# Optimization experiments

Measured on AMD Instinct MI355X. Metric: run time of the kernel, lower is better.

## Reference

```python
import jax, jax.numpy as jnp
import numpy as np

K = 10  # num_neighbors in original nn_index call


def setup_inputs() -> dict:
    key = jax.random.key(0)
    k1, k2, k3, k4 = jax.random.split(key, 4)
    B, OBS, ACT, N = 256, 32, 2, 500000
    obs = jax.random.normal(k1, (B, OBS), dtype=jnp.float32)
    action = jax.random.normal(k2, (B, ACT), dtype=jnp.float32)
    mem_sa = jax.random.normal(k3, (N, OBS + ACT), dtype=jnp.float32)
    mem_Q = jax.random.normal(k4, (N, 1), dtype=jnp.float32)
    return {"obs": obs, "action": action, "mem_sa": mem_sa, "mem_Q": mem_Q}


def reference(obs, action, mem_sa, mem_Q):
    # query: [B, D] state-action, brute-force kNN over memory table [N, D]
    q = jnp.concatenate([obs, action], axis=1)
    # squared Euclidean distances (FLANN returns squared L2): [B, N]
    d2 = (jnp.sum(q * q, axis=1, keepdims=True)
          - 2.0 * q @ mem_sa.T
          + jnp.sum(mem_sa * mem_sa, axis=1)[None, :])
    neg_d, idx = jax.lax.top_k(-d2, K)   # nearest K neighbors
    dists = -neg_d                        # [B, K], ascending
    Qs = mem_Q[idx, 0]                    # gather Q values: [B, K]
    # NOTE: original applies softmax to raw distances (not negated)
    weights = jax.nn.softmax(dists, axis=1)
    return jnp.sum(weights * Qs, axis=1)  # [B]
```

## Files before the change

### kernel.cpp

```cpp
#include <hip/hip_runtime.h>
#include <hip/hip_bf16.h>
#include <math.h>

#define NPTS   500000
#define NB     256
#define TOPK   10
#define CAP    2048
#define SBLK   1024
#define SPER   16
#define MARGIN 2.0f
#define NWCH   15625
#define FBLK   512
#define NSEG   2
#define LCAP   8
#define PMAIN  393216
#define OCAP   32768

typedef short v2s  __attribute__((ext_vector_type(2)));
typedef short v4s  __attribute__((ext_vector_type(4)));
typedef short v8s  __attribute__((ext_vector_type(8)));
typedef float v16f __attribute__((ext_vector_type(16)));

__device__ __forceinline__ unsigned short f2bf(float f) {
    unsigned u = __float_as_uint(f);
    unsigned r = u + 0x7FFFu + ((u >> 16) & 1u);
    return (unsigned short)(r >> 16);
}
__device__ __forceinline__ float bf2f(unsigned short h) {
    return __uint_as_float(((unsigned)h) << 16);
}
__device__ __forceinline__ v2s pk2(float2 f) {
    __hip_bfloat162 h = __float22bfloat162_rn(f);
    v2s r;
    __builtin_memcpy(&r, &h, 4);
    return r;
}

__device__ __forceinline__ float norm34(const float* __restrict__ r) {
    float a0 = 0.f, a1 = 0.f, a2 = 0.f, a3 = 0.f;
#pragma unroll
    for (int d = 0; d < 32; d += 4) {
        a0 = fmaf(r[d + 0], r[d + 0], a0);
        a1 = fmaf(r[d + 1], r[d + 1], a1);
        a2 = fmaf(r[d + 2], r[d + 2], a2);
        a3 = fmaf(r[d + 3], r[d + 3], a3);
    }
    a0 = fmaf(r[32], r[32], a0);
    a1 = fmaf(r[33], r[33], a1);
    return (a0 + a1) + (a2 + a3);
}
__device__ __forceinline__ float dot34(const float* __restrict__ r, const float* q) {
    float a0 = 0.f, a1 = 0.f, a2 = 0.f, a3 = 0.f;
#pragma unroll
    for (int d = 0; d < 32; d += 4) {
        a0 = fmaf(r[d + 0], q[d + 0], a0);
        a1 = fmaf(r[d + 1], q[d + 1], a1);
        a2 = fmaf(r[d + 2], q[d + 2], a2);
        a3 = fmaf(r[d + 3], q[d + 3], a3);
    }
    a0 = fmaf(r[32], q[32], a0);
    a1 = fmaf(r[33], q[33], a1);
    return (a0 + a1) + (a2 + a3);
}
__device__ __forceinline__ float dot34_v4(const float4* __restrict__ r4, const float* q) {
    float a0 = 0.f, a1 = 0.f, a2 = 0.f, a3 = 0.f;
#pragma unroll
    for (int dp = 0; dp < 8; ++dp) {
        float4 v = r4[dp];
        a0 = fmaf(v.x, q[4 * dp + 0], a0);
        a1 = fmaf(v.y, q[4 * dp + 1], a1);
        a2 = fmaf(v.z, q[4 * dp + 2], a2);
        a3 = fmaf(v.w, q[4 * dp + 3], a3);
    }
    float2 t = *(const float2*)(r4 + 8);
    a0 = fmaf(t.x, q[32], a0);
    a1 = fmaf(t.y, q[33], a1);
    return (a0 + a1) + (a2 + a3);
}
__device__ __forceinline__ void load_q(const float* __restrict__ obs,
                                       const float* __restrict__ act, int b, float* q) {
#pragma unroll
    for (int d = 0; d < 32; ++d) q[d] = obs[b * 32 + d];
    q[32] = act[b * 2 + 0];
    q[33] = act[b * 2 + 1];
}
__device__ __forceinline__ void load9(float2* __restrict__ e,
                                      const float* __restrict__ rp, int half) {
    e[0] = *(const float2*)(rp + half * 8 + 0);
    e[1] = *(const float2*)(rp + half * 8 + 2);
    e[2] = *(const float2*)(rp + half * 8 + 4);
    e[3] = *(const float2*)(rp + half * 8 + 6);
    e[4] = *(const float2*)(rp + 16 + half * 8 + 0);
    e[5] = *(const float2*)(rp + 16 + half * 8 + 2);
    e[6] = *(const float2*)(rp + 16 + half * 8 + 4);
    e[7] = *(const float2*)(rp + 16 + half * 8 + 6);
    e[8] = *(const float2*)(rp + 32);
}

__global__ __launch_bounds__(256, 4) void k_sample(const float* __restrict__ obs,
                                                   const float* __restrict__ act,
                                                   const float* __restrict__ msa,
                                                   float* __restrict__ minima) {
    __shared__ __align__(16) float sm[SPER * 36];
    __shared__ float smn[SPER];
    const int g = blockIdx.x, t = threadIdx.x;
    const int base = g * SPER;
    for (int i = t; i < SPER * 34; i += 256) {
        int row = i / 34, d = i - row * 34;
        sm[row * 36 + d] = msa[(size_t)base * 34 + i];
    }
    __syncthreads();
    if (t < SPER) smn[t] = norm34(&sm[t * 36]);
    __syncthreads();
    float q[34];
    load_q(obs, act, t, q);
    float best = __builtin_inff();
#pragma unroll
    for (int j = 0; j < SPER; ++j) {
        float s = fmaf(-2.f, dot34_v4((const float4*)&sm[j * 36], q), smn[j]);
        best = fminf(best, s);
    }
    minima[(size_t)t * SBLK + g] = best;
}

__global__ __launch_bounds__(64) void k_tau(const float* __restrict__ minima,
                                            const float* __restrict__ obs,
                                            const float* __restrict__ act,
                                            v8s* __restrict__ afrag,
                                            int* __restrict__ cursor) {
    __shared__ __align__(16) unsigned short qs[48];
    const int b = blockIdx.x, lane = threadIdx.x;
    if (b == 0 && lane == 0) { cursor[0] = 0; cursor[1] = 0; }
    float v[16];
#pragma unroll
    for (int k = 0; k < 16; ++k) v[k] = minima[(size_t)b * SBLK + lane + 64 * k];
    float last = 0.f;
    for (int r = 0; r < TOPK; ++r) {
        float lm = v[0]; int la = 0;
#pragma unroll
        for (int k = 1; k < 16; ++k) { if (v[k] < lm) { lm = v[k]; la = k; } }
        float wm = lm;
        for (int off = 32; off; off >>= 1) wm = fminf(wm, __shfl_xor(wm, off));
        unsigned long long msk = __ballot(lm == wm);
        int first = (int)__builtin_ctzll(msk);
        if (lane == first) {
#pragma unroll
            for (int k = 0; k < 16; ++k) { if (k == la) v[k] = __builtin_inff(); }
        }
        last = wm;
    }
    float val = 0.f;
    if (lane < 32)       val = obs[b * 32 + lane];
    else if (lane < 34)  val = act[b * 2 + (lane - 32)];
    else if (lane == 34) val = -0.5f;
    else if (lane == 35) val = 0.5f * (last + MARGIN);
    if (lane < 48) qs[lane] = (lane < 36) ? f2bf(val) : (unsigned short)0;
    __syncthreads();
    if (lane < 6) {
        int s = lane >> 1, half = lane & 1;
        int qt = b >> 5, mrow = b & 31;
        v8s frag = *(const v8s*)&qs[s * 16 + half * 8];
        afrag[(qt * 3 + s) * 64 + half * 32 + mrow] = frag;
    }
}

__global__ __launch_bounds__(256, 2) void k_filter(const float* __restrict__ msa,
                                                   const v8s* __restrict__ afrag,
                                                   int* __restrict__ cursor,
                                                   unsigned* __restrict__ pbuf,
                                                   int* __restrict__ posq) {
    __shared__ int lcount[NB];
    __shared__ int lcand[NB * LCAP];
    __shared__ int gbase;
    const int g = blockIdx.x, t = threadIdx.x;
    const int w = t >> 6, lane = t & 63;
    const int mrow = lane & 31, half = lane >> 5;
    v8s A[8][3];
#pragma unroll
    for (int qt = 0; qt < 8; ++qt)
#pragma unroll
        for (int s = 0; s < 3; ++s)
            A[qt][s] = afrag[(qt * 3 + s) * 64 + lane];
    lcount[t] = 0;
    __syncthreads();
    const v16f zacc = (v16f)0.0f;
    const int gw = g * 4 + w;
    const int step = FBLK * 4;

    auto process = [&](const float2* c, int wc) {
        const int p0 = wc * 32 + mrow;
        float n0 = 0.f, n1 = 0.f;
        n0 = fmaf(c[0].x, c[0].x, n0); n1 = fmaf(c[0].y, c[0].y, n1);
        n0 = fmaf(c[1].x, c[1].x, n0); n1 = fmaf(c[1].y, c[1].y, n1);
        n0 = fmaf(c[2].x, c[2].x, n0); n1 = fmaf(c[2].y, c[2].y, n1);
        n0 = fmaf(c[3].x, c[3].x, n0); n1 = fmaf(c[3].y, c[3].y, n1);
        n0 = fmaf(c[4].x, c[4].x, n0); n1 = fmaf(c[4].y, c[4].y, n1);
        n0 = fmaf(c[5].x, c[5].x, n0); n1 = fmaf(c[5].y, c[5].y, n1);
        n0 = fmaf(c[6].x, c[6].x, n0); n1 = fmaf(c[6].y, c[6].y, n1);
        n0 = fmaf(c[7].x, c[7].x, n0); n1 = fmaf(c[7].y, c[7].y, n1);
        float part = n0 + n1;
        part = fmaf(c[8].x, c[8].x * 0.5f, part);
        part = fmaf(c[8].y, c[8].y * 0.5f, part);
        float nrm = part + __shfl_xor(part, 32);
        float thr = 0.5f * nrm;
        v4s b0lo = __builtin_shufflevector(pk2(c[0]), pk2(c[1]), 0, 1, 2, 3);
        v4s b0hi = __builtin_shufflevector(pk2(c[2]), pk2(c[3]), 0, 1, 2, 3);
        v8s B0 = __builtin_shufflevector(b0lo, b0hi, 0, 1, 2, 3, 4, 5, 6, 7);
        v4s b1lo = __builtin_shufflevector(pk2(c[4]), pk2(c[5]), 0, 1, 2, 3);
        v4s b1hi = __builtin_shufflevector(pk2(c[6]), pk2(c[7]), 0, 1, 2, 3);
        v8s B1 = __builtin_shufflevector(b1lo, b1hi, 0, 1, 2, 3, 4, 5, 6, 7);
        v8s B2 = (v8s)(short)0;
        if (half == 0) {
            v2s m33 = pk2(c[8]);
            B2[0] = m33[0];
            B2[1] = m33[1];
            B2[3] = (short)0x3F80;
        }
#pragma unroll
        for (int qt = 0; qt < 8; ++qt) {
            v16f acc = __builtin_amdgcn_mfma_f32_32x32x16_bf16(A[qt][0], B0, zacc, 0, 0, 0);
            acc = __builtin_amdgcn_mfma_f32_32x32x16_bf16(A[qt][1], B1, acc, 0, 0, 0);
            acc = __builtin_amdgcn_mfma_f32_32x32x16_bf16(A[qt][2], B2, acc, 0, 0, 0);
            float m0 = fmaxf(fmaxf(acc[0], acc[1]), acc[2]);
            float m1 = fmaxf(fmaxf(acc[3], acc[4]), acc[5]);
            float m2 = fmaxf(fmaxf(acc[6], acc[7]), acc[8]);
            float m3 = fmaxf(fmaxf(acc[9], acc[10]), acc[11]);
            float m4 = fmaxf(fmaxf(acc[12], acc[13]), acc[14]);
            float mx = fmaxf(fmaxf(fmaxf(m0, m1), m2),
                             fmaxf(fmaxf(m3, m4), acc[15]));
            if (mx >= thr) {
                unsigned hm = 0;
#pragma unroll
                for (int r = 0; r < 16; ++r) hm |= (acc[r] >= thr) ? (1u << r) : 0u;
                while (hm) {
                    int r = __builtin_ctz(hm);
                    hm &= hm - 1;
                    int qq = qt * 32 + (r & 3) + 8 * (r >> 2) + 4 * half;
                    int slot = atomicAdd(&lcount[qq], 1);
                    if (slot < LCAP) lcand[qq * LCAP + slot] = p0;
                    else {
                        int dg = atomicAdd(cursor + 1, 1);
                        if (dg < OCAP) pbuf[PMAIN + dg] = ((unsigned)qq << 19) | (unsigned)p0;
                    }
                }
            }
        }
    };

    float2 bufA[9], bufB[9];
    int wc = gw;
    load9(bufA, msa + (size_t)(wc * 32 + mrow) * 34, half);
#pragma unroll 1
    for (;;) {
        const int w1 = wc + step;
        {
            const int pn = (w1 < NWCH) ? w1 : gw;
            load9(bufB, msa + (size_t)(pn * 32 + mrow) * 34, half);
        }
        __builtin_amdgcn_sched_barrier(0);
        process(bufA, wc);
        wc = w1;
        if (wc >= NWCH) break;
        const int w2 = wc + step;
        {
            const int pn = (w2 < NWCH) ? w2 : gw;
            load9(bufA, msa + (size_t)(pn * 32 + mrow) * 34, half);
        }
        __builtin_amdgcn_sched_barrier(0);
        process(bufB, wc);
        wc = w2;
        if (wc >= NWCH) break;
    }
    __syncthreads();
    int n = lcount[t];
    if (n > LCAP) n = LCAP;
    lcount[t] = n;
    __syncthreads();
    for (int off = 1; off < 256; off <<= 1) {
        int v = (t >= off) ? lcount[t - off] : 0;
        __syncthreads();
        lcount[t] += v;
        __syncthreads();
    }
    int base_l = lcount[t] - n;
    if (t == 255) gbase = atomicAdd(cursor, lcount[255]);
    __syncthreads();
    int start = gbase + base_l;
    if (start >= PMAIN) { start = 0; n = 0; }
    else if (start + n > PMAIN) n = PMAIN - start;
    posq[g * NB + t] = start | (n << 20);
    for (int i = 0; i < n; ++i)
        pbuf[start + i] = (unsigned)lcand[t * LCAP + i];
}

__global__ __launch_bounds__(256) void k_final(const float* __restrict__ obs,
                                               const float* __restrict__ act,
                                               const float* __restrict__ msa,
                                               const unsigned* __restrict__ pbuf,
                                               const int* __restrict__ posq,
                                               const int* __restrict__ cursor,
                                               const float* __restrict__ memQ,
                                               float* __restrict__ out) {
    __shared__ float ls[CAP];
    __shared__ int   li[CAP];
    __shared__ int   sc[NB];
    __shared__ int   lcnt;
    __shared__ float rs[4];
    __shared__ int   ri[4];
    __shared__ float sel_s[TOPK];
    __shared__ int   sel_i[TOPK];
    const int b = blockIdx.x, t = threadIdx.x;
    const int lane = t & 63, wid = t >> 6;
    int nk[NSEG], pk6[NSEG], tot = 0;
#pragma unroll
    for (int k = 0; k < NSEG; ++k) {
        int packed = posq[(size_t)(t + 256 * k) * NB + b];
        nk[k] = (packed >> 20) & 0xF;
        pk6[k] = packed & 0xFFFFF;
        tot += nk[k];
    }
    sc[t] = tot;
    __syncthreads();
    for (int off = 1; off < 256; off <<= 1) {
        int v = (t >= off) ? sc[t - off] : 0;
        __syncthreads();
        sc[t] += v;
        __syncthreads();
    }
    int myoff = sc[t] - tot;
    if (t == 0) lcnt = (sc[255] > CAP) ? CAP : sc[255];
    __syncthreads();
#pragma unroll
    for (int k = 0; k < NSEG; ++k)
        for (int i = 0; i < nk[k]; ++i) {
            if (myoff < CAP) li[myoff] = (int)pbuf[pk6[k] + i];
            ++myoff;
        }
    int novf = cursor[1];
    if (novf > OCAP) novf = OCAP;
    for (int j = t; j < novf; j += 256) {
        unsigned pr = pbuf[PMAIN + j];
        if ((int)(pr >> 19) == b) {
            int s = atomicAdd(&lcnt, 1);
            if (s < CAP) li[s] = (int)(pr & 0x7FFFFu);
        }
    }
    __syncthreads();
    int cnt = lcnt;
    if (cnt > CAP) cnt = CAP;
    float q[34];
    load_q(obs, act, b, q);
    for (int j = t; j < cnt; j += 256) {
        const float* row = msa + (size_t)li[j] * 34;
        ls[j] = fmaf(-2.f, dot34(row, q), norm34(row));
    }
    __syncthreads();
    for (int k = 0; k < TOPK; ++k) {
        float bs = __builtin_inff();
        int   bi = 0x7fffffff;
        for (int j = t; j < cnt; j += 256) {
            float s = ls[j]; int i = li[j];
            if (s < bs || (s == bs && i < bi)) { bs = s; bi = i; }
        }
        for (int off = 32; off; off >>= 1) {
            float s2 = __shfl_down(bs, off);
            int   i2 = __shfl_down(bi, off);
            if (s2 < bs || (s2 == bs && i2 < bi)) { bs = s2; bi = i2; }
        }
        if (lane == 0) { rs[wid] = bs; ri[wid] = bi; }
        __syncthreads();
        if (t == 0) {
            float fs = rs[0]; int fi = ri[0];
#pragma unroll
            for (int ww = 1; ww < 4; ++ww) {
                if (rs[ww] < fs || (rs[ww] == fs && ri[ww] < fi)) { fs = rs[ww]; fi = ri[ww]; }
            }
            sel_s[k] = fs; sel_i[k] = fi;
        }
        __syncthreads();
        const int win = sel_i[k];
        for (int j = t; j < cnt; j += 256) {
            if (li[j] == win) ls[j] = __builtin_inff();
        }
        __syncthreads();
    }
    if (t == 0) {
        float m = sel_s[TOPK - 1];
        float wsum = 0.f, acc = 0.f;
#pragma unroll
        for (int k = 0; k < TOPK; ++k) {
            if (sel_i[k] == 0x7fffffff) continue;
            float w2 = expf(sel_s[k] - m);
            wsum += w2;
            acc = fmaf(w2, memQ[sel_i[k]], acc);
        }
        out[b] = acc / wsum;
    }
}

extern "C" void kernel_launch(void* const* d_in, const int* in_sizes, int n_in,
                              void* d_out, int out_size, void* d_ws, size_t ws_size,
                              hipStream_t stream) {
    const float* obs = (const float*)d_in[0];
    const float* act = (const float*)d_in[1];
    const float* msa = (const float*)d_in[2];
    const float* mq  = (const float*)d_in[3];
    float* out = (float*)d_out;

    char* ws = (char*)d_ws;
    int*      cursor = (int*)ws;
    v8s*      afrag  = (v8s*)(ws + 256);
    float*    minima = (float*)(ws + 32768);
    int*      posq   = (int*)(ws + 32768 + 1048576);
    unsigned* pbuf   = (unsigned*)(ws + 32768 + 1048576 + 1572864);

    k_sample<<<SBLK, 256, 0, stream>>>(obs, act, msa, minima);
    k_tau   <<<NB, 64, 0, stream>>>(minima, obs, act, afrag, cursor);
    k_filter<<<FBLK, 256, 0, stream>>>(msa, afrag, cursor, pbuf, posq);
    k_final <<<NB, 256, 0, stream>>>(obs, act, msa, pbuf, posq, cursor, mq, out);
}
```

Measured before the change: 168.1 us.

## Fuse four kernels into one persistent megakernel with grid-wide barriers

Merges the sample, tau, filter and final kernels into a single persistent kernel of 512 blocks that separates phases with atomic-counter grid barriers, plus a tiny init kernel that zeroes the counters. Each block now handles two sample slices so the 1024 slices fit the smaller grid. The aim is to remove the launch gaps and tail drain between the four dependent launches. In exchange it adds spin-wait barrier cost and relies on all 512 blocks being co-resident, since otherwise the barriers deadlock. Only half the blocks do useful work in the tau and final phases.

Result: slower. 306.2 us (+82.2%).

```diff
diff --git a/kernel.cpp b/kernel.cpp
--- a/kernel.cpp
+++ b/kernel.cpp
@@ -6,11 +6,11 @@
 #define NB     256
 #define TOPK   10
 #define CAP    2048
+#define GRID   512
 #define SBLK   1024
 #define SPER   16
 #define MARGIN 2.0f
 #define NWCH   15625
-#define FBLK   512
 #define NSEG   2
 #define LCAP   8
 #define PMAIN  393216
@@ -25,9 +25,6 @@
     unsigned u = __float_as_uint(f);
     unsigned r = u + 0x7FFFu + ((u >> 16) & 1u);
     return (unsigned short)(r >> 16);
-}
-__device__ __forceinline__ float bf2f(unsigned short h) {
-    return __uint_as_float(((unsigned)h) << 16);
 }
 __device__ __forceinline__ v2s pk2(float2 f) {
     __hip_bfloat162 h = __float22bfloat162_rn(f);
@@ -97,304 +94,321 @@
     e[8] = *(const float2*)(rp + 32);
 }
 
-__global__ __launch_bounds__(256, 4) void k_sample(const float* __restrict__ obs,
-                                                   const float* __restrict__ act,
-                                                   const float* __restrict__ msa,
-                                                   float* __restrict__ minima) {
-    __shared__ __align__(16) float sm[SPER * 36];
-    __shared__ float smn[SPER];
+__device__ __forceinline__ void gsync(int* cnt) {
+    __syncthreads();
+    if (threadIdx.x == 0) {
+        __threadfence();
+        atomicAdd(cnt, 1);
+        while (atomicAdd(cnt, 0) < GRID) __builtin_amdgcn_s_sleep(2);
+        __threadfence();
+    }
+    __syncthreads();
+}
+
+struct SmSample { float sm[SPER * 36]; float smn[SPER]; };
+struct SmTau    { unsigned short qs[48]; };
+struct SmFilter { int lcount[NB]; int lcand[NB * LCAP]; int gbase; };
+struct SmFinal  { float ls[CAP]; int li[CAP]; int sc[NB]; int lcnt;
+                  float rs[4]; int ri[4];
+                  float sel_s[TOPK]; int sel_i[TOPK]; };
+
+__global__ void k_init(int* wsi) {
+    const int t = threadIdx.x;
+    if (t < 64) wsi[t] = 0;
+}
+
+__global__ __launch_bounds__(256, 2) void k_mega(const float* __restrict__ obs,
+                                                 const float* __restrict__ act,
+                                                 const float* __restrict__ msa,
+                                                 const float* __restrict__ memQ,
+                                                 int* __restrict__ cursor,
+                                                 int* __restrict__ bars,
+                                                 v8s* __restrict__ afrag,
+                                                 float* __restrict__ minima,
+                                                 int* __restrict__ posq,
+                                                 unsigned* __restrict__ pbuf,
+                                                 float* __restrict__ out) {
+    __shared__ __align__(16) char smraw[17536];
     const int g = blockIdx.x, t = threadIdx.x;
-    const int base = g * SPER;
-    for (int i = t; i < SPER * 34; i += 256) {
-        int row = i / 34, d = i - row * 34;
-        sm[row * 36 + d] = msa[(size_t)base * 34 + i];
-    }
-    __syncthreads();
-    if (t < SPER) smn[t] = norm34(&sm[t * 36]);
-    __syncthreads();
-    float q[34];
-    load_q(obs, act, t, q);
-    float best = __builtin_inff();
-#pragma unroll
-    for (int j = 0; j < SPER; ++j) {
-        float s = fmaf(-2.f, dot34_v4((const float4*)&sm[j * 36], q), smn[j]);
-        best = fminf(best, s);
-    }
-    minima[(size_t)t * SBLK + g] = best;
-}
-
-__global__ __launch_bounds__(64) void k_tau(const float* __restrict__ minima,
-                                            const float* __restrict__ obs,
-                                            const float* __restrict__ act,
-                                            v8s* __restrict__ afrag,
-                                            int* __restrict__ cursor) {
-    __shared__ __align__(16) unsigned short qs[48];
-    const int b = blockIdx.x, lane = threadIdx.x;
-    if (b == 0 && lane == 0) { cursor[0] = 0; cursor[1] = 0; }
-    float v[16];
-#pragma unroll
-    for (int k = 0; k < 16; ++k) v[k] = minima[(size_t)b * SBLK + lane + 64 * k];
-    float last = 0.f;
-    for (int r = 0; r < TOPK; ++r) {
-        float lm = v[0]; int la = 0;
-#pragma unroll
-        for (int k = 1; k < 16; ++k) { if (v[k] < lm) { lm = v[k]; la = k; } }
-        float wm = lm;
-        for (int off = 32; off; off >>= 1) wm = fminf(wm, __shfl_xor(wm, off));
-        unsigned long long msk = __ballot(lm == wm);
-        int first = (int)__builtin_ctzll(msk);
-        if (lane == first) {
-#pragma unroll
-            for (int k = 0; k < 16; ++k) { if (k == la) v[k] = __builtin_inff(); }
-        }
-        last = wm;
-    }
-    float val = 0.f;
-    if (lane < 32)       val = obs[b * 32 + lane];
-    else if (lane < 34)  val = act[b * 2 + (lane - 32)];
-    else if (lane == 34) val = -0.5f;
-    else if (lane == 35) val = 0.5f * (last + MARGIN);
-    if (lane < 48) qs[lane] = (lane < 36) ? f2bf(val) : (unsigned short)0;
-    __syncthreads();
-    if (lane < 6) {
-        int s = lane >> 1, half = lane & 1;
-        int qt = b >> 5, mrow = b & 31;
-        v8s frag = *(const v8s*)&qs[s * 16 + half * 8];
-        afrag[(qt * 3 + s) * 64 + half * 32 + mrow] = frag;
-    }
-}
-
-__global__ __launch_bounds__(256, 2) void k_filter(const float* __restrict__ msa,
-                                                   const v8s* __restrict__ afrag,
-                                                   int* __restrict__ cursor,
-                                                   unsigned* __restrict__ pbuf,
-                                                   int* __restrict__ posq) {
-    __shared__ int lcount[NB];
-    __shared__ int lcand[NB * LCAP];
-    __shared__ int gbase;
-    const int g = blockIdx.x, t = threadIdx.x;
-    const int w = t >> 6, lane = t & 63;
-    const int mrow = lane & 31, half = lane >> 5;
-    v8s A[8][3];
-#pragma unroll
-    for (int qt = 0; qt < 8; ++qt)
-#pragma unroll
-        for (int s = 0; s < 3; ++s)
-            A[qt][s] = afrag[(qt * 3 + s) * 64 + lane];
-    lcount[t] = 0;
-    __syncthreads();
-    const v16f zacc = (v16f)0.0f;
-    const int gw = g * 4 + w;
-    const int step = FBLK * 4;
-
-    auto process = [&](const float2* c, int wc) {
-        const int p0 = wc * 32 + mrow;
-        float n0 = 0.f, n1 = 0.f;
-        n0 = fmaf(c[0].x, c[0].x, n0); n1 = fmaf(c[0].y, c[0].y, n1);
-        n0 = fmaf(c[1].x, c[1].x, n0); n1 = fmaf(c[1].y, c[1].y, n1);
-        n0 = fmaf(c[2].x, c[2].x, n0); n1 = fmaf(c[2].y, c[2].y, n1);
-        n0 = fmaf(c[3].x, c[3].x, n0); n1 = fmaf(c[3].y, c[3].y, n1);
-        n0 = fmaf(c[4].x, c[4].x, n0); n1 = fmaf(c[4].y, c[4].y, n1);
-        n0 = fmaf(c[5].x, c[5].x, n0); n1 = fmaf(c[5].y, c[5].y, n1);
-        n0 = fmaf(c[6].x, c[6].x, n0); n1 = fmaf(c[6].y, c[6].y, n1);
-        n0 = fmaf(c[7].x, c[7].x, n0); n1 = fmaf(c[7].y, c[7].y, n1);
-        float part = n0 + n1;
-        part = fmaf(c[8].x, c[8].x * 0.5f, part);
-        part = fmaf(c[8].y, c[8].y * 0.5f, part);
-        float nrm = part + __shfl_xor(part, 32);
-        float thr = 0.5f * nrm;
-        v4s b0lo = __builtin_shufflevector(pk2(c[0]), pk2(c[1]), 0, 1, 2, 3);
-        v4s b0hi = __builtin_shufflevector(pk2(c[2]), pk2(c[3]), 0, 1, 2, 3);
-        v8s B0 = __builtin_shufflevector(b0lo, b0hi, 0, 1, 2, 3, 4, 5, 6, 7);
-        v4s b1lo = __builtin_shufflevector(pk2(c[4]), pk2(c[5]), 0, 1, 2, 3);
-        v4s b1hi = __builtin_shufflevector(pk2(c[6]), pk2(c[7]), 0, 1, 2, 3);
-        v8s B1 = __builtin_shufflevector(b1lo, b1hi, 0, 1, 2, 3, 4, 5, 6, 7);
-        v8s B2 = (v8s)(short)0;
-        if (half == 0) {
-            v2s m33 = pk2(c[8]);
-            B2[0] = m33[0];
-            B2[1] = m33[1];
-            B2[3] = (short)0x3F80;
-        }
-#pragma unroll
-        for (int qt = 0; qt < 8; ++qt) {
-            v16f acc = __builtin_amdgcn_mfma_f32_32x32x16_bf16(A[qt][0], B0, zacc, 0, 0, 0);
-            acc = __builtin_amdgcn_mfma_f32_32x32x16_bf16(A[qt][1], B1, acc, 0, 0, 0);
-            acc = __builtin_amdgcn_mfma_f32_32x32x16_bf16(A[qt][2], B2, acc, 0, 0, 0);
-            float m0 = fmaxf(fmaxf(acc[0], acc[1]), acc[2]);
-            float m1 = fmaxf(fmaxf(acc[3], acc[4]), acc[5]);
-            float m2 = fmaxf(fmaxf(acc[6], acc[7]), acc[8]);
-            float m3 = fmaxf(fmaxf(acc[9], acc[10]), acc[11]);
-            float m4 = fmaxf(fmaxf(acc[12], acc[13]), acc[14]);
-            float mx = fmaxf(fmaxf(fmaxf(m0, m1), m2),
-                             fmaxf(fmaxf(m3, m4), acc[15]));
-            if (mx >= thr) {
-                unsigned hm = 0;
-#pragma unroll
-                for (int r = 0; r < 16; ++r) hm |= (acc[r] >= thr) ? (1u << r) : 0u;
-                while (hm) {
-                    int r = __builtin_ctz(hm);
-                    hm &= hm - 1;
-                    int qq = qt * 32 + (r & 3) + 8 * (r >> 2) + 4 * half;
-                    int slot = atomicAdd(&lcount[qq], 1);
-                    if (slot < LCAP) lcand[qq * LCAP + slot] = p0;
-                    else {
-                        int dg = atomicAdd(cursor + 1, 1);
-                        if (dg < OCAP) pbuf[PMAIN + dg] = ((unsigned)qq << 19) | (unsigned)p0;
+
+    {
+        SmSample& S = *reinterpret_cast<SmSample*>(smraw);
+        float q[34];
+        load_q(obs, act, t, q);
+#pragma unroll 1
+        for (int sl = 0; sl < 2; ++sl) {
+            const int slice = g * 2 + sl;
+            const int base = slice * SPER;
+            for (int i = t; i < SPER * 34; i += 256) {
+                int row = i / 34, d = i - row * 34;
+                S.sm[row * 36 + d] = msa[(size_t)base * 34 + i];
+            }
+            __syncthreads();
+            if (t < SPER) S.smn[t] = norm34(&S.sm[t * 36]);
+            __syncthreads();
+            float best = __builtin_inff();
+#pragma unroll
+            for (int j = 0; j < SPER; ++j) {
+                float s = fmaf(-2.f, dot34_v4((const float4*)&S.sm[j * 36], q), S.smn[j]);
+                best = fminf(best, s);
+            }
+            minima[(size_t)t * SBLK + slice] = best;
+            __syncthreads();
+        }
+    }
+    gsync(bars + 0);
+
+    if (g < NB) {
+        SmTau& T = *reinterpret_cast<SmTau*>(smraw);
+        if (t < 64) {
+            const int lane = t;
+            float v[16];
+#pragma unroll
+            for (int k = 0; k < 16; ++k) v[k] = minima[(size_t)g * SBLK + lane + 64 * k];
+            float last = 0.f;
+            for (int r = 0; r < TOPK; ++r) {
+                float lm = v[0]; int la = 0;
+#pragma unroll
+                for (int k = 1; k < 16; ++k) { if (v[k] < lm) { lm = v[k]; la = k; } }
+                float wm = lm;
+                for (int off = 32; off; off >>= 1) wm = fminf(wm, __shfl_xor(wm, off));
+                unsigned long long msk = __ballot(lm == wm);
+                int first = (int)__builtin_ctzll(msk);
+                if (lane == first) {
+#pragma unroll
+                    for (int k = 0; k < 16; ++k) { if (k == la) v[k] = __builtin_inff(); }
+                }
+                last = wm;
+            }
+            float val = 0.f;
+            if (lane < 32)       val = obs[g * 32 + lane];
+            else if (lane < 34)  val = act[g * 2 + (lane - 32)];
+            else if (lane == 34) val = -0.5f;
+            else if (lane == 35) val = 0.5f * (last + MARGIN);
+            if (lane < 48) T.qs[lane] = (lane < 36) ? f2bf(val) : (unsigned short)0;
+        }
+        __syncthreads();
+        if (t < 6) {
+            int s = t >> 1, half = t & 1;
+            int qt = g >> 5, mrow = g & 31;
+            v8s frag = *(const v8s*)&T.qs[s * 16 + half * 8];
+            afrag[(qt * 3 + s) * 64 + half * 32 + mrow] = frag;
+        }
+    }
+    gsync(bars + 1);
+
+    {
+        SmFilter& F = *reinterpret_cast<SmFilter*>(smraw);
+        const int w = t >> 6, lane = t & 63;
+        const int mrow = lane & 31, half = lane >> 5;
+        v8s A[8][3];
+#pragma unroll
+        for (int qt = 0; qt < 8; ++qt)
+#pragma unroll
+            for (int s = 0; s < 3; ++s)
+                A[qt][s] = afrag[(qt * 3 + s) * 64 + lane];
+        F.lcount[t] = 0;
+        __syncthreads();
+        const v16f zacc = (v16f)0.0f;
+        const int gw = g * 4 + w;
+        const int step = GRID * 4;
+
+        auto process = [&](const float2* c, int wc) {
+            const int p0 = wc * 32 + mrow;
+            float n0 = 0.f, n1 = 0.f;
+            n0 = fmaf(c[0].x, c[0].x, n0); n1 = fmaf(c[0].y, c[0].y, n1);
+            n0 = fmaf(c[1].x, c[1].x, n0); n1 = fmaf(c[1].y, c[1].y, n1);
+            n0 = fmaf(c[2].x, c[2].x, n0); n1 = fmaf(c[2].y, c[2].y, n1);
+            n0 = fmaf(c[3].x, c[3].x, n0); n1 = fmaf(c[3].y, c[3].y, n1);
+            n0 = fmaf(c[4].x, c[4].x, n0); n1 = fmaf(c[4].y, c[4].y, n1);
+            n0 = fmaf(c[5].x, c[5].x, n0); n1 = fmaf(c[5].y, c[5].y, n1);
+            n0 = fmaf(c[6].x, c[6].x, n0); n1 = fmaf(c[6].y, c[6].y, n1);
+            n0 = fmaf(c[7].x, c[7].x, n0); n1 = fmaf(c[7].y, c[7].y, n1);
+            float part = n0 + n1;
+            part = fmaf(c[8].x, c[8].x * 0.5f, part);
+            part = fmaf(c[8].y, c[8].y * 0.5f, part);
+            float nrm = part + __shfl_xor(part, 32);
+            float thr = 0.5f * nrm;
+            v4s b0lo = __builtin_shufflevector(pk2(c[0]), pk2(c[1]), 0, 1, 2, 3);
+            v4s b0hi = __builtin_shufflevector(pk2(c[2]), pk2(c[3]), 0, 1, 2, 3);
+            v8s B0 = __builtin_shufflevector(b0lo, b0hi, 0, 1, 2, 3, 4, 5, 6, 7);
+            v4s b1lo = __builtin_shufflevector(pk2(c[4]), pk2(c[5]), 0, 1, 2, 3);
+            v4s b1hi = __builtin_shufflevector(pk2(c[6]), pk2(c[7]), 0, 1, 2, 3);
+            v8s B1 = __builtin_shufflevector(b1lo, b1hi, 0, 1, 2, 3, 4, 5, 6, 7);
+            v8s B2 = (v8s)(short)0;
+            if (half == 0) {
+                v2s m33 = pk2(c[8]);
+                B2[0] = m33[0];
+                B2[1] = m33[1];
+                B2[3] = (short)0x3F80;
+            }
+#pragma unroll
+            for (int qt = 0; qt < 8; ++qt) {
+                v16f acc = __builtin_amdgcn_mfma_f32_32x32x16_bf16(A[qt][0], B0, zacc, 0, 0, 0);
+                acc = __builtin_amdgcn_mfma_f32_32x32x16_bf16(A[qt][1], B1, acc, 0, 0, 0);
+                acc = __builtin_amdgcn_mfma_f32_32x32x16_bf16(A[qt][2], B2, acc, 0, 0, 0);
+                float m0 = fmaxf(fmaxf(acc[0], acc[1]), acc[2]);
+                float m1 = fmaxf(fmaxf(acc[3], acc[4]), acc[5]);
+                float m2 = fmaxf(fmaxf(acc[6], acc[7]), acc[8]);
+                float m3 = fmaxf(fmaxf(acc[9], acc[10]), acc[11]);
+                float m4 = fmaxf(fmaxf(acc[12], acc[13]), acc[14]);
+                float mx = fmaxf(fmaxf(fmaxf(m0, m1), m2),
+                                 fmaxf(fmaxf(m3, m4), acc[15]));
+                if (mx >= thr) {
+                    unsigned hm = 0;
+#pragma unroll
+                    for (int r = 0; r < 16; ++r) hm |= (acc[r] >= thr) ? (1u << r) : 0u;
+                    while (hm) {
+                        int r = __builtin_ctz(hm);
+                        hm &= hm - 1;
+                        int qq = qt * 32 + (r & 3) + 8 * (r >> 2) + 4 * half;
+                        int slot = atomicAdd(&F.lcount[qq], 1);
+                        if (slot < LCAP) F.lcand[qq * LCAP + slot] = p0;
+                        else {
+                            int dg = atomicAdd(cursor + 1, 1);
+                            if (dg < OCAP) pbuf[PMAIN + dg] = ((unsigned)qq << 19) | (unsigned)p0;
+                        }
                     }
                 }
             }
-        }
-    };
-
-    float2 bufA[9], bufB[9];
-    int wc = gw;
-    load9(bufA, msa + (size_t)(wc * 32 + mrow) * 34, half);
+        };
+
+        float2 bufA[9], bufB[9];
+        int wc = gw;
+        load9(bufA, msa + (size_t)(wc * 32 + mrow) * 34, half);
 #pragma unroll 1
-    for (;;) {
-        const int w1 = wc + step;
-        {
-            const int pn = (w1 < NWCH) ? w1 : gw;
-            load9(bufB, msa + (size_t)(pn * 32 + mrow) * 34, half);
-        }
-        __builtin_amdgcn_sched_barrier(0);
-        process(bufA, wc);
-        wc = w1;
-        if (wc >= NWCH) break;
-        const int w2 = wc + step;
-        {
-            const int pn = (w2 < NWCH) ? w2 : gw;
-            load9(bufA, msa + (size_t)(pn * 32 + mrow) * 34, half);
-        }
-        __builtin_amdgcn_sched_barrier(0);
-        process(bufB, wc);
-        wc = w2;
-        if (wc >= NWCH) break;
-    }
-    __syncthreads();
-    int n = lcount[t];
-    if (n > LCAP) n = LCAP;
-    lcount[t] = n;
-    __syncthreads();
-    for (int off = 1; off < 256; off <<= 1) {
-        int v = (t >= off) ? lcount[t - off] : 0;
-        __syncthreads();
-        lcount[t] += v;
-        __syncthreads();
-    }
-    int base_l = lcount[t] - n;
-    if (t == 255) gbase = atomicAdd(cursor, lcount[255]);
-    __syncthreads();
-    int start = gbase + base_l;
-    if (start >= PMAIN) { start = 0; n = 0; }
-    else if (start + n > PMAIN) n = PMAIN - start;
-    posq[g * NB + t] = start | (n << 20);
-    for (int i = 0; i < n; ++i)
-        pbuf[start + i] = (unsigned)lcand[t * LCAP + i];
-}
-
-__global__ __launch_bounds__(256) void k_final(const float* __restrict__ obs,
-                                               const float* __restrict__ act,
-                                               const float* __restrict__ msa,
-                                               const unsigned* __restrict__ pbuf,
-                                               const int* __restrict__ posq,
-                                               const int* __restrict__ cursor,
-                                               const float* __restrict__ memQ,
-                                               float* __restrict__ out) {
-    __shared__ float ls[CAP];
-    __shared__ int   li[CAP];
-    __shared__ int   sc[NB];
-    __shared__ int   lcnt;
-    __shared__ float rs[4];
-    __shared__ int   ri[4];
-    __shared__ float sel_s[TOPK];
-    __shared__ int   sel_i[TOPK];
-    const int b = blockIdx.x, t = threadIdx.x;
-    const int lane = t & 63, wid = t >> 6;
-    int nk[NSEG], pk6[NSEG], tot = 0;
-#pragma unroll
-    for (int k = 0; k < NSEG; ++k) {
-        int packed = posq[(size_t)(t + 256 * k) * NB + b];
-        nk[k] = (packed >> 20) & 0xF;
-        pk6[k] = packed & 0xFFFFF;
-        tot += nk[k];
-    }
-    sc[t] = tot;
-    __syncthreads();
-    for (int off = 1; off < 256; off <<= 1) {
-        int v = (t >= off) ? sc[t - off] : 0;
-        __syncthreads();
-        sc[t] += v;
-        __syncthreads();
-    }
-    int myoff = sc[t] - tot;
-    if (t == 0) lcnt = (sc[255] > CAP) ? CAP : sc[255];
-    __syncthreads();
-#pragma unroll
-    for (int k = 0; k < NSEG; ++k)
-        for (int i = 0; i < nk[k]; ++i) {
-            if (myoff < CAP) li[myoff] = (int)pbuf[pk6[k] + i];
-            ++myoff;
-        }
-    int novf = cursor[1];
-    if (novf > OCAP) novf = OCAP;
-    for (int j = t; j < novf; j += 256) {
-        unsigned pr = pbuf[PMAIN + j];
-        if ((int)(pr >> 19) == b) {
-            int s = atomicAdd(&lcnt, 1);
-            if (s < CAP) li[s] = (int)(pr & 0x7FFFFu);
-        }
-    }
-    __syncthreads();
-    int cnt = lcnt;
-    if (cnt > CAP) cnt = CAP;
-    float q[34];
-    load_q(obs, act, b, q);
-    for (int j = t; j < cnt; j += 256) {
-        const float* row = msa + (size_t)li[j] * 34;
-        ls[j] = fmaf(-2.f, dot34(row, q), norm34(row));
-    }
-    __syncthreads();
-    for (int k = 0; k < TOPK; ++k) {
-        float bs = __builtin_inff();
-        int   bi = 0x7fffffff;
+        for (;;) {
+            const int w1 = wc + step;
+            {
+                const int pn = (w1 < NWCH) ? w1 : gw;
+                load9(bufB, msa + (size_t)(pn * 32 + mrow) * 34, half);
+            }
+            __builtin_amdgcn_sched_barrier(0);
+            process(bufA, wc);
+            wc = w1;
+            if (wc >= NWCH) break;
+            const int w2 = wc + step;
+            {
+                const int pn = (w2 < NWCH) ? w2 : gw;
+                load9(bufA, msa + (size_t)(pn * 32 + mrow) * 34, half);
+            }
+            __builtin_amdgcn_sched_barrier(0);
+            process(bufB, wc);
+            wc = w2;
+            if (wc >= NWCH) break;
+        }
+        __syncthreads();
+        int n = F.lcount[t];
+        if (n > LCAP) n = LCAP;
+        F.lcount[t] = n;
+        __syncthreads();
+        for (int off = 1; off < 256; off <<= 1) {
+            int v = (t >= off) ? F.lcount[t - off] : 0;
+            __syncthreads();
+            F.lcount[t] += v;
+            __syncthreads();
+        }
+        int base_l = F.lcount[t] - n;
+        if (t == 255) F.gbase = atomicAdd(cursor, F.lcount[255]);
+        __syncthreads();
+        int start = F.gbase + base_l;
+        if (start >= PMAIN) { start = 0; n = 0; }
+        else if (start + n > PMAIN) n = PMAIN - start;
+        posq[g * NB + t] = start | (n << 20);
+        for (int i = 0; i < n; ++i)
+            pbuf[start + i] = (unsigned)F.lcand[t * LCAP + i];
+    }
+    gsync(bars + 2);
+
+    if (g < NB) {
+        SmFinal& F = *reinterpret_cast<SmFinal*>(smraw);
+        const int b = g;
+        const int lane = t & 63, wid = t >> 6;
+        int nk[NSEG], pk6[NSEG], tot = 0;
+#pragma unroll
+        for (int k = 0; k < NSEG; ++k) {
+            int packed = posq[(size_t)(t + 256 * k) * NB + b];
+            nk[k] = (packed >> 20) & 0xF;
+            pk6[k] = packed & 0xFFFFF;
+            tot += nk[k];
+        }
+        F.sc[t] = tot;
+        __syncthreads();
+        for (int off = 1; off < 256; off <<= 1) {
+            int v = (t >= off) ? F.sc[t - off] : 0;
+            __syncthreads();
+            F.sc[t] += v;
+            __syncthreads();
+        }
+        int myoff = F.sc[t] - tot;
+        if (t == 0) F.lcnt = (F.sc[255] > CAP) ? CAP : F.sc[255];
+        __syncthreads();
+#pragma unroll
+        for (int k = 0; k < NSEG; ++k)
+            for (int i = 0; i < nk[k]; ++i) {
+                if (myoff < CAP) F.li[myoff] = (int)pbuf[pk6[k] + i];
+                ++myoff;
+            }
+        int novf = cursor[1];
+        if (novf > OCAP) novf = OCAP;
+        for (int j = t; j < novf; j += 256) {
+            unsigned pr = pbuf[PMAIN + j];
+            if ((int)(pr >> 19) == b) {
+                int s = atomicAdd(&F.lcnt, 1);
+                if (s < CAP) F.li[s] = (int)(pr & 0x7FFFFu);
+            }
+        }
+        __syncthreads();
+        int cnt = F.lcnt;
+        if (cnt > CAP) cnt = CAP;
+        float q[34];
+        load_q(obs, act, b, q);
         for (int j = t; j < cnt; j += 256) {
-            float s = ls[j]; int i = li[j];
-            if (s < bs || (s == bs && i < bi)) { bs = s; bi = i; }
-        }
-        for (int off = 32; off; off >>= 1) {
-            float s2 = __shfl_down(bs, off);
-            int   i2 = __shfl_down(bi, off);
-            if (s2 < bs || (s2 == bs && i2 < bi)) { bs = s2; bi = i2; }
-        }
-        if (lane == 0) { rs[wid] = bs; ri[wid] = bi; }
-        __syncthreads();
+            const float* row = msa + (size_t)F.li[j] * 34;
+            F.ls[j] = fmaf(-2.f, dot34(row, q), norm34(row));
+        }
+        __syncthreads();
+        for (int k = 0; k < TOPK; ++k) {
+            float bs = __builtin_inff();
+            int   bi = 0x7fffffff;
+            for (int j = t; j < cnt; j += 256) {
+                float s = F.ls[j]; int i = F.li[j];
+                if (s < bs || (s == bs && i < bi)) { bs = s; bi = i; }
+            }
+            for (int off = 32; off; off >>= 1) {
+                float s2 = __shfl_down(bs, off);
+                int   i2 = __shfl_down(bi, off);
+                if (s2 < bs || (s2 == bs && i2 < bi)) { bs = s2; bi = i2; }
+            }
+            if (lane == 0) { F.rs[wid] = bs; F.ri[wid] = bi; }
+            __syncthreads();
+            if (t == 0) {
+                float fs = F.rs[0]; int fi = F.ri[0];
+#pragma unroll
+                for (int ww = 1; ww < 4; ++ww) {
+                    if (F.rs[ww] < fs || (F.rs[ww] == fs && F.ri[ww] < fi)) { fs = F.rs[ww]; fi = F.ri[ww]; }
+                }
+                F.sel_s[k] = fs; F.sel_i[k] = fi;
+            }
+            __syncthreads();
+            const int win = F.sel_i[k];
+            for (int j = t; j < cnt; j += 256) {
+                if (F.li[j] == win) F.ls[j] = __builtin_inff();
+            }
+            __syncthreads();
+        }
         if (t == 0) {
-            float fs = rs[0]; int fi = ri[0];
-#pragma unroll
-            for (int ww = 1; ww < 4; ++ww) {
-                if (rs[ww] < fs || (rs[ww] == fs && ri[ww] < fi)) { fs = rs[ww]; fi = ri[ww]; }
-            }
-            sel_s[k] = fs; sel_i[k] = fi;
-        }
-        __syncthreads();
-        const int win = sel_i[k];
-        for (int j = t; j < cnt; j += 256) {
-            if (li[j] == win) ls[j] = __builtin_inff();
-        }
-        __syncthreads();
-    }
-    if (t == 0) {
-        float m = sel_s[TOPK - 1];
-        float wsum = 0.f, acc = 0.f;
-#pragma unroll
-        for (int k = 0; k < TOPK; ++k) {
-            if (sel_i[k] == 0x7fffffff) continue;
-            float w2 = expf(sel_s[k] - m);
-            wsum += w2;
-            acc = fmaf(w2, memQ[sel_i[k]], acc);
-        }
-        out[b] = acc / wsum;
+            float m = F.sel_s[TOPK - 1];
+            float wsum = 0.f, acc = 0.f;
+#pragma unroll
+            for (int k = 0; k < TOPK; ++k) {
+                if (F.sel_i[k] == 0x7fffffff) continue;
+                float w2 = expf(F.sel_s[k] - m);
+                wsum += w2;
+                acc = fmaf(w2, memQ[F.sel_i[k]], acc);
+            }
+            out[b] = acc / wsum;
+        }
     }
 }
 
@@ -408,14 +422,15 @@
     float* out = (float*)d_out;
 
     char* ws = (char*)d_ws;
+    int*      wsi    = (int*)ws;
     int*      cursor = (int*)ws;
+    int*      bars   = (int*)(ws + 64);
     v8s*      afrag  = (v8s*)(ws + 256);
     float*    minima = (float*)(ws + 32768);
     int*      posq   = (int*)(ws + 32768 + 1048576);
     unsigned* pbuf   = (unsigned*)(ws + 32768 + 1048576 + 1572864);
 
-    k_sample<<<SBLK, 256, 0, stream>>>(obs, act, msa, minima);
-    k_tau   <<<NB, 64, 0, stream>>>(minima, obs, act, afrag, cursor);
-    k_filter<<<FBLK, 256, 0, stream>>>(msa, afrag, cursor, pbuf, posq);
-    k_final <<<NB, 256, 0, stream>>>(obs, act, msa, pbuf, posq, cursor, mq, out);
-}
+    k_init<<<1, 64, 0, stream>>>(wsi);
+    k_mega<<<GRID, 256, 0, stream>>>(obs, act, msa, mq, cursor, bars,
+                                     afrag, minima, posq, pbuf, out);
+}
```
